# Kernel optimization log

Hardware: AMD Instinct MI355X
Metric: run time of the kernel (lower is better)

Reference implementation:

```python
import jax, jax.numpy as jnp
import numpy as np

K_RATIO = 0.5
NUM_CLASSES = 5
NUM_QUERIES = 96


def setup_inputs() -> dict:
    key = jax.random.key(0)
    kA, kX, kW = jax.random.split(key, 3)
    B, N, D = 4, 4096, 128
    A = jax.random.uniform(kA, (B, N, N), dtype=jnp.float32)
    X = jax.random.normal(kX, (B, N, D), dtype=jnp.float32)
    W = jax.random.normal(kW, (D, 1), dtype=jnp.float32) * (1.0 / np.sqrt(D))
    b = jnp.zeros((1,), dtype=jnp.float32)
    return {"A": A, "X": X, "W": W, "b": b}


def reference(A, X, W, b):
    # pool_mode == 'way' branch of GraphPool, vectorized over batch and classes.
    B, N, D = X.shape
    S = (N - NUM_QUERIES) // NUM_CLASSES      # supports per class
    kk = int(K_RATIO * S)                      # kept per class
    # per-node score: sigmoid(Linear(X)/100)   [B, N]
    scores = jax.nn.sigmoid((jnp.einsum('bnd,do->bn', X, W) + b[0]) / 100.0)
    # per-class top-k over support segments
    sup = scores[:, :NUM_CLASSES * S].reshape(B, NUM_CLASSES, S)
    way_vals, way_idx = jax.lax.top_k(sup, kk)                 # [B, C, kk]
    way_idx = (way_idx + (jnp.arange(NUM_CLASSES) * S)[None, :, None]).reshape(B, -1)
    way_vals = way_vals.reshape(B, -1)
    # queries are always kept
    q_idx = jnp.broadcast_to(jnp.arange(N - NUM_QUERIES, N)[None, :], (B, NUM_QUERIES))
    idx = jnp.concatenate([way_idx, q_idx], axis=1)            # [B, newN]
    vals = jnp.concatenate([way_vals, scores[:, N - NUM_QUERIES:]], axis=1)
    # gather features, scale by scores
    new_X = jnp.take_along_axis(X, idx[:, :, None], axis=1) * vals[:, :, None]
    # double-indexed adjacency gather A[idx][:, idx]
    bidx = jnp.arange(B)[:, None, None]
    new_A = A[bidx, idx[:, :, None], idx[:, None, :]]          # [B, newN, newN]
    return new_A, new_X, idx
```

## Files before the change

kernel.cpp:

```cpp
#include <hip/hip_runtime.h>
#include <math.h>

#define BB   4
#define NN   4096
#define DD   128
#define NCLS 5
#define SS   800
#define KK   400
#define NQ   96
#define MM   (NCLS*KK + NQ)
#define NSUP (NCLS*SS)

__global__ void score_kernel(const float* __restrict__ X, const float* __restrict__ W,
                             const float* __restrict__ bias,
                             float* __restrict__ scoreF) {
    int row  = blockIdx.x * 4 + (threadIdx.x >> 6);
    int lane = threadIdx.x & 63;
    if (row >= BB * NN) return;
    const float* x = X + (size_t)row * DD;
    double acc = (double)x[lane]      * (double)W[lane]
               + (double)x[lane + 64] * (double)W[lane + 64];
    #pragma unroll
    for (int off = 32; off > 0; off >>= 1) acc += __shfl_down(acc, off);
    if (lane == 0) {
        float z32 = (float)acc;
        float u   = (z32 + bias[0]) / 100.0f;
        float e   = (float)exp(-(double)u);
        float t   = 1.0f + e;
        float s   = 1.0f / t;
        scoreF[row] = s;
    }
}

__global__ void __launch_bounds__(1024)
topk_kernel(const float* __restrict__ scoreF, int* __restrict__ gidx, float* __restrict__ gvals) {
    __shared__ unsigned long long buf[2][1024];
    const int b = blockIdx.x / NCLS;
    const int c = blockIdx.x % NCLS;
    const int t = threadIdx.x;

    if (c == 0 && t >= 512 && t < 512 + NQ) {
        int q  = t - 512;
        int gi = NSUP + q;
        int m  = NCLS * KK + q;
        gidx [b * MM + m] = gi;
        gvals[b * MM + m] = scoreF[(size_t)b * NN + gi];
    }

    const float* sc = scoreF + (size_t)b * NN + c * SS;
    unsigned long long v = 0ull;
    if (t < SS)
        v = ((unsigned long long)__float_as_uint(sc[t]) << 32) | (unsigned int)(1023 - t);

    int p = 0;
    for (int k = 2; k <= 1024; k <<= 1) {
        for (int j = k >> 1; j > 0; j >>= 1) {
            unsigned long long o;
            if (j >= 64) {
                buf[p][t] = v;
                __syncthreads();
                o = buf[p][t ^ j];
                p ^= 1;
            } else {
                unsigned int lo = __shfl_xor((unsigned int)(v & 0xFFFFFFFFu), j);
                unsigned int hi = __shfl_xor((unsigned int)(v >> 32), j);
                o = ((unsigned long long)hi << 32) | lo;
            }
            bool keepMax = (((t & k) == 0) == ((t & j) == 0));
            v = keepMax ? (v > o ? v : o) : (v < o ? v : o);
        }
    }

    if (t < KK) {
        int li = 1023 - (int)(v & 0xFFFFFFFFull);
        gidx [b * MM + c * KK + t] = c * SS + li;
        gvals[b * MM + c * KK + t] = __uint_as_float((unsigned int)(v >> 32));
    }
}

__global__ void __launch_bounds__(256)
newxa_kernel(const float* __restrict__ A, const float* __restrict__ X,
             const int* __restrict__ gidx, const float* __restrict__ gvals,
             float* __restrict__ outA, float* __restrict__ outX, float* __restrict__ outIdx) {
    __shared__ int cidx[MM];
    const int bm = blockIdx.x;
    const int b  = bm / MM;
    const int* gb = gidx + b * MM;
    for (int j = threadIdx.x; j < MM; j += 256) cidx[j] = gb[j];
    __syncthreads();

    const int ri = cidx[bm - b * MM];

    if (threadIdx.x < DD) {
        float vscale = gvals[bm];
        outX[(size_t)bm * DD + threadIdx.x] =
            X[((size_t)b * NN + ri) * DD + threadIdx.x] * vscale;
        if (threadIdx.x == 0) outIdx[bm] = (float)ri;
    }

    const float* arow = A + ((size_t)b * NN + ri) * NN;
    float* orow = outA + (size_t)bm * MM;
    for (int jj = threadIdx.x * 4; jj < MM; jj += 1024) {
        float4 vv;
        vv.x = arow[cidx[jj]];
        vv.y = arow[cidx[jj + 1]];
        vv.z = arow[cidx[jj + 2]];
        vv.w = arow[cidx[jj + 3]];
        *(float4*)(orow + jj) = vv;
    }
}

extern "C" void kernel_launch(void* const* d_in, const int* in_sizes, int n_in,
                              void* d_out, int out_size, void* d_ws, size_t ws_size,
                              hipStream_t stream) {
    const float* A  = (const float*)d_in[0];
    const float* X  = (const float*)d_in[1];
    const float* W  = (const float*)d_in[2];
    const float* bi = (const float*)d_in[3];

    float* outA   = (float*)d_out;
    float* outX   = outA + (size_t)BB * MM * MM;
    float* outIdx = outX + (size_t)BB * MM * DD;

    char* ws = (char*)d_ws;
    float* scoreF = (float*)ws;
    int*   gidx   = (int*)  (ws + 65536);
    float* gvals  = (float*)(ws + 65536 + 33536);

    score_kernel<<<(BB * NN) / 4, 256, 0, stream>>>(X, W, bi, scoreF);
    topk_kernel<<<BB * NCLS, 1024, 0, stream>>>(scoreF, gidx, gvals);
    newxa_kernel<<<BB * MM, 256, 0, stream>>>(A, X, gidx, gvals, outA, outX, outIdx);
}
```

Baseline: 57.97 us.

## Fuse score into topk and stage full A rows in LDS for gather

Removes the separate score kernel by computing each node's sigmoid score inside the top-k block, with each thread doing a full 128-wide dot product from vectorized loads against W held in shared memory. The adjacency gather now streams the entire 4096-float A row into LDS with nontemporal vector loads, then does the indexed gather from LDS, and outputs use nontemporal stores. This saves one launch and replaces scattered global reads with coalesced ones. In exchange it reads the whole row (about 2x the needed bytes), adds 16KB of LDS per block, and the score step runs on only 20 blocks with per-thread serial dot products.

Result: slower. 65.67 us (+13.3%).

```diff
diff --git a/kernel.cpp b/kernel.cpp
--- a/kernel.cpp
+++ b/kernel.cpp
@@ -11,46 +11,51 @@
 #define MM   (NCLS*KK + NQ)
 #define NSUP (NCLS*SS)
 
-__global__ void score_kernel(const float* __restrict__ X, const float* __restrict__ W,
-                             const float* __restrict__ bias,
-                             float* __restrict__ scoreF) {
-    int row  = blockIdx.x * 4 + (threadIdx.x >> 6);
-    int lane = threadIdx.x & 63;
-    if (row >= BB * NN) return;
-    const float* x = X + (size_t)row * DD;
-    double acc = (double)x[lane]      * (double)W[lane]
-               + (double)x[lane + 64] * (double)W[lane + 64];
-    #pragma unroll
-    for (int off = 32; off > 0; off >>= 1) acc += __shfl_down(acc, off);
-    if (lane == 0) {
-        float z32 = (float)acc;
-        float u   = (z32 + bias[0]) / 100.0f;
-        float e   = (float)exp(-(double)u);
-        float t   = 1.0f + e;
-        float s   = 1.0f / t;
-        scoreF[row] = s;
-    }
-}
+typedef float f4 __attribute__((ext_vector_type(4)));
 
 __global__ void __launch_bounds__(1024)
-topk_kernel(const float* __restrict__ scoreF, int* __restrict__ gidx, float* __restrict__ gvals) {
+topk_kernel(const float* __restrict__ X, const float* __restrict__ W,
+            const float* __restrict__ bias,
+            int* __restrict__ gidx, float* __restrict__ gvals) {
     __shared__ unsigned long long buf[2][1024];
+    __shared__ float Ws[DD];
     const int b = blockIdx.x / NCLS;
     const int c = blockIdx.x % NCLS;
     const int t = threadIdx.x;
 
-    if (c == 0 && t >= 512 && t < 512 + NQ) {
-        int q  = t - 512;
-        int gi = NSUP + q;
-        int m  = NCLS * KK + q;
-        gidx [b * MM + m] = gi;
-        gvals[b * MM + m] = scoreF[(size_t)b * NN + gi];
+    if (t < DD) Ws[t] = W[t];
+    __syncthreads();
+
+    float s = 0.0f;
+    int row = -1;
+    if (t < SS) row = c * SS + t;
+    else if (c == 0 && t < SS + NQ) row = NSUP + (t - SS);
+    if (row >= 0) {
+        const f4* x4 = (const f4*)(X + ((size_t)b * NN + row) * DD);
+        double acc = 0.0;
+        #pragma unroll
+        for (int i = 0; i < DD / 4; ++i) {
+            f4 xv = x4[i];
+            acc += (double)xv.x * (double)Ws[4*i]
+                 + (double)xv.y * (double)Ws[4*i+1]
+                 + (double)xv.z * (double)Ws[4*i+2]
+                 + (double)xv.w * (double)Ws[4*i+3];
+        }
+        float z32 = (float)acc;
+        float u   = (z32 + bias[0]) / 100.0f;
+        float e   = (float)exp(-(double)u);
+        s = 1.0f / (1.0f + e);
     }
 
-    const float* sc = scoreF + (size_t)b * NN + c * SS;
+    if (c == 0 && t >= SS && t < SS + NQ) {
+        int q = t - SS;
+        gidx [b * MM + NCLS * KK + q] = NSUP + q;
+        gvals[b * MM + NCLS * KK + q] = s;
+    }
+
     unsigned long long v = 0ull;
     if (t < SS)
-        v = ((unsigned long long)__float_as_uint(sc[t]) << 32) | (unsigned int)(1023 - t);
+        v = ((unsigned long long)__float_as_uint(s) << 32) | (unsigned int)(1023 - t);
 
     int p = 0;
     for (int k = 2; k <= 1024; k <<= 1) {
@@ -82,7 +87,8 @@
 newxa_kernel(const float* __restrict__ A, const float* __restrict__ X,
              const int* __restrict__ gidx, const float* __restrict__ gvals,
              float* __restrict__ outA, float* __restrict__ outX, float* __restrict__ outIdx) {
-    __shared__ int cidx[MM];
+    __shared__ int   cidx[MM];
+    __shared__ float rowA[NN];
     const int bm = blockIdx.x;
     const int b  = bm / MM;
     const int* gb = gidx + b * MM;
@@ -91,22 +97,30 @@
 
     const int ri = cidx[bm - b * MM];
 
+    const f4* arow4 = (const f4*)(A + ((size_t)b * NN + ri) * NN);
+    f4* rowA4 = (f4*)rowA;
+    #pragma unroll
+    for (int j = 0; j < NN / 4 / 256; ++j) {
+        int p = j * 256 + threadIdx.x;
+        rowA4[p] = __builtin_nontemporal_load(arow4 + p);
+    }
+
     if (threadIdx.x < DD) {
         float vscale = gvals[bm];
-        outX[(size_t)bm * DD + threadIdx.x] =
-            X[((size_t)b * NN + ri) * DD + threadIdx.x] * vscale;
+        float xv = X[((size_t)b * NN + ri) * DD + threadIdx.x] * vscale;
+        __builtin_nontemporal_store(xv, outX + (size_t)bm * DD + threadIdx.x);
         if (threadIdx.x == 0) outIdx[bm] = (float)ri;
     }
+    __syncthreads();
 
-    const float* arow = A + ((size_t)b * NN + ri) * NN;
     float* orow = outA + (size_t)bm * MM;
     for (int jj = threadIdx.x * 4; jj < MM; jj += 1024) {
-        float4 vv;
-        vv.x = arow[cidx[jj]];
-        vv.y = arow[cidx[jj + 1]];
-        vv.z = arow[cidx[jj + 2]];
-        vv.w = arow[cidx[jj + 3]];
-        *(float4*)(orow + jj) = vv;
+        f4 vv;
+        vv.x = rowA[cidx[jj]];
+        vv.y = rowA[cidx[jj + 1]];
+        vv.z = rowA[cidx[jj + 2]];
+        vv.w = rowA[cidx[jj + 3]];
+        __builtin_nontemporal_store(vv, (f4*)(orow + jj));
     }
 }
 
@@ -123,11 +137,9 @@
     float* outIdx = outX + (size_t)BB * MM * DD;
 
     char* ws = (char*)d_ws;
-    float* scoreF = (float*)ws;
-    int*   gidx   = (int*)  (ws + 65536);
-    float* gvals  = (float*)(ws + 65536 + 33536);
+    int*   gidx  = (int*)  ws;
+    float* gvals = (float*)(ws + 33536);
 
-    score_kernel<<<(BB * NN) / 4, 256, 0, stream>>>(X, W, bi, scoreF);
-    topk_kernel<<<BB * NCLS, 1024, 0, stream>>>(scoreF, gidx, gvals);
+    topk_kernel<<<BB * NCLS, 1024, 0, stream>>>(X, W, bi, gidx, gvals);
     newxa_kernel<<<BB * MM, 256, 0, stream>>>(A, X, gidx, gvals, outA, outX, outIdx);
 }
```
